# Kernel tuning notes

Hardware: AMD Instinct MI355X
Metric: run time of the kernel (lower is better)

Reference implementation:

```python
import jax, jax.numpy as jnp
import numpy as np

N = 10                 # n_wires
DIM = 1 << N           # Hilbert space dim = 1024
OPS = [''.join('Z' if i == j else 'I' for i in range(N)) for j in range(N)] + \
      [p + 'I' * (N - 2) for p in ['XX', 'YY', 'ZZ', 'XY', 'XZ', 'YZ']]

C64 = jnp.complex64
CNOT = jnp.array([[1, 0, 0, 0], [0, 1, 0, 0], [0, 0, 0, 1], [0, 0, 1, 0]], dtype=C64)
PAULI = {'X': jnp.array([[0, 1], [1, 0]], dtype=C64),
         'Y': jnp.array([[0, -1j], [1j, 0]], dtype=C64),
         'Z': jnp.array([[1, 0], [0, -1]], dtype=C64)}


def _rx(theta):
    c = jnp.cos(theta / 2).astype(C64)
    s = jnp.sin(theta / 2).astype(C64)
    return jnp.stack([jnp.stack([c, -1j * s]), jnp.stack([-1j * s, c])])


def _ry(theta):
    c = jnp.cos(theta / 2).astype(C64)
    s = jnp.sin(theta / 2).astype(C64)
    return jnp.stack([jnp.stack([c, -s]), jnp.stack([s, c])])


def _apply_gate(U, gate, qubits):
    """Left-multiply U by gate expanded onto `qubits` (little-endian: qubit 0 = LSB
    of the row index), without materializing the 2^N x 2^N expanded operator.
    Equivalent to expand_operator(gate, qubits, N) @ U."""
    k = len(qubits)
    T = U.reshape((2,) * N + (DIM,))          # row bit b <-> axis N-1-b
    src = tuple(N - 1 - q for q in reversed(qubits))  # MSB of gate index first
    T = jnp.moveaxis(T, src, tuple(range(k)))
    shp = T.shape
    T = (gate @ T.reshape(1 << k, -1)).reshape(shp)
    T = jnp.moveaxis(T, tuple(range(k)), src)
    return T.reshape(DIM, DIM)


def _build_unitary(rx0, ry0, ry1):
    U = jnp.eye(DIM, dtype=C64)
    for j in range(N):                         # local RY0 @ RX0 on each qubit
        U = _apply_gate(U, _ry(ry0[j]) @ _rx(rx0[j]), [j])
    for _ in range(N):                         # N entangling layers
        for j in range(N):
            U = _apply_gate(U, CNOT, [j, (j + 1) % N])
        for j in range(N):
            U = _apply_gate(U, _ry(ry1[j]), [j])
    return U


def _apply_pauli(states, p, q):
    """states: (BT,) + (2,)*N with qubit q at axis 1 + (N-1-q)."""
    ax = 1 + (N - 1 - q)
    s = jnp.moveaxis(states, ax, -1)
    s = jnp.einsum('ab,...b->...a', p, s)
    return jnp.moveaxis(s, -1, ax)


def setup_inputs() -> dict:
    key = jax.random.key(0)
    kx, k1, k2, k3 = jax.random.split(key, 4)
    x = jax.random.normal(kx, (16, 1024, 1024), dtype=jnp.float32)
    pi = np.float32(np.pi)
    rx0 = jax.random.uniform(k1, (N,), minval=-pi, maxval=pi, dtype=jnp.float32)
    ry0 = jax.random.uniform(k2, (N,), minval=-pi, maxval=pi, dtype=jnp.float32)
    ry1 = jax.random.uniform(k3, (N,), minval=-pi, maxval=pi, dtype=jnp.float32)
    return {"x": x, "rx0": rx0, "ry0": ry0, "ry1": ry1}


def reference(x, rx0, ry0, ry1):
    B, T, C = x.shape
    U = _build_unitary(rx0, ry0, ry1)
    xf = x.reshape(B * T, C)
    # amplitude encoding: L2-normalize each row onto the 2^N state
    psi = (xf / jnp.linalg.norm(xf, axis=-1, keepdims=True)).astype(C64)
    psi_out = psi @ U.T                        # (BT, DIM)
    phi0 = psi_out.reshape((B * T,) + (2,) * N)
    evs = []
    for op in OPS:
        phi = phi0
        for q, ch in enumerate(op):
            if ch != 'I':
                phi = _apply_pauli(phi, PAULI[ch], q)
        evs.append(jnp.sum(jnp.real(jnp.conj(phi0) * phi),
                           axis=tuple(range(1, N + 1))))
    out = jnp.stack(evs, axis=-1)              # (BT, hidden_dim)
    return out.reshape(B, T, len(OPS)).astype(jnp.float32)
```

## Files before the change

### kernel.cpp

```cpp
#include <hip/hip_runtime.h>

#define DIM 1024

typedef _Float16 half8  __attribute__((ext_vector_type(8)));
typedef _Float16 half4v __attribute__((ext_vector_type(4)));
typedef float    f32x4  __attribute__((ext_vector_type(4)));

#define LO_SCALE   2048.0f
#define LO_INV     4.8828125e-4f

__device__ __forceinline__ int swz(int p) { return p ^ ((p >> 4) & 15); }

__device__ __forceinline__ void gl2lds(const _Float16* g, _Float16* s) {
  __builtin_amdgcn_global_load_lds(
      (const __attribute__((address_space(1))) void*)g,
      (__attribute__((address_space(3))) void*)s, 16, 0, 0);
}

__global__ __launch_bounds__(256) void k_build(
    const float* __restrict__ rx0, const float* __restrict__ ry0,
    const float* __restrict__ ry1, _Float16* __restrict__ BtH,
    _Float16* __restrict__ BtL) {
  __shared__ float2 st[2][4][DIM];
  __shared__ unsigned short invp[DIM];
  __shared__ float2 rot[30];
  const int t = threadIdx.x;
  const int w = t >> 6;
  const int l = t & 63;
  const int k0 = blockIdx.x * 4;

  if (t < 30) {
    float th = (t < 10) ? rx0[t] : (t < 20 ? ry0[t - 10] : ry1[t - 20]);
    rot[t] = make_float2(cosf(0.5f * th), sinf(0.5f * th));
  }
  for (int p = t; p < DIM; p += 256) {
    int b = p;
    #pragma unroll
    for (int j = 9; j >= 0; --j) b ^= ((b >> ((j + 1) % 10)) & 1) << j;
    invp[p] = (unsigned short)b;
  }
  {
    const int k = k0 + w;
    for (int i = 0; i < 16; ++i) {
      int p = l * 16 + i;
      st[0][w][swz(p)] = make_float2(p == k ? 1.f : 0.f, 0.f);
    }
  }
  __syncthreads();

  int cur = 0;

  auto quad = [&](int qbase, bool ph1, bool gather) {
    float2 v[16];
    #pragma unroll
    for (int i = 0; i < 16; ++i) {
      int p = (qbase == 0) ? ((l << 4) | i)
                           : (((l >> 4) << 8) | (i << 4) | (l & 15));
      int sp = gather ? (int)invp[p] : p;
      v[i] = st[cur][w][swz(sp)];
    }
    #pragma unroll
    for (int qq = 0; qq < 4; ++qq) {
      const int q = qbase + qq;
      if (ph1) {
        const float cx = rot[q].x, sx = rot[q].y;
        #pragma unroll
        for (int i = 0; i < 16; ++i) {
          if (i & (1 << qq)) continue;
          const int j = i | (1 << qq);
          float2 a = v[i], b = v[j];
          v[i] = make_float2(cx*a.x + sx*b.y,  cx*a.y - sx*b.x);
          v[j] = make_float2(sx*a.y + cx*b.x, -sx*a.x + cx*b.y);
        }
      }
      const float cy = ph1 ? rot[10+q].x : rot[20+q].x;
      const float sy = ph1 ? rot[10+q].y : rot[20+q].y;
      #pragma unroll
      for (int i = 0; i < 16; ++i) {
        if (i & (1 << qq)) continue;
        const int j = i | (1 << qq);
        float2 a = v[i], b = v[j];
        v[i] = make_float2(cy*a.x - sy*b.x, cy*a.y - sy*b.y);
        v[j] = make_float2(sy*a.x + cy*b.x, sy*a.y + cy*b.y);
      }
    }
    const int dst = gather ? (cur ^ 1) : cur;
    #pragma unroll
    for (int i = 0; i < 16; ++i) {
      int p = (qbase == 0) ? ((l << 4) | i)
                           : (((l >> 4) << 8) | (i << 4) | (l & 15));
      st[dst][w][swz(p)] = v[i];
    }
    if (gather) cur ^= 1;
    __syncthreads();
  };

  auto duo = [&](bool ph1) {
    #pragma unroll
    for (int rep = 0; rep < 4; ++rep) {
      const int u = l + rep * 64;
      float2 v[4];
      #pragma unroll
      for (int i = 0; i < 4; ++i) v[i] = st[cur][w][swz((i << 8) | u)];
      #pragma unroll
      for (int qq = 0; qq < 2; ++qq) {
        const int q = 8 + qq;
        if (ph1) {
          const float cx = rot[q].x, sx = rot[q].y;
          #pragma unroll
          for (int i = 0; i < 4; ++i) {
            if (i & (1 << qq)) continue;
            const int j = i | (1 << qq);
            float2 a = v[i], b = v[j];
            v[i] = make_float2(cx*a.x + sx*b.y,  cx*a.y - sx*b.x);
            v[j] = make_float2(sx*a.y + cx*b.x, -sx*a.x + cx*b.y);
          }
        }
        const float cy = ph1 ? rot[10+q].x : rot[20+q].x;
        const float sy = ph1 ? rot[10+q].y : rot[20+q].y;
        #pragma unroll
        for (int i = 0; i < 4; ++i) {
          if (i & (1 << qq)) continue;
          const int j = i | (1 << qq);
          float2 a = v[i], b = v[j];
          v[i] = make_float2(cy*a.x - sy*b.x, cy*a.y - sy*b.y);
          v[j] = make_float2(sy*a.x + cy*b.x, sy*a.y + cy*b.y);
        }
      }
      #pragma unroll
      for (int i = 0; i < 4; ++i) st[cur][w][swz((i << 8) | u)] = v[i];
    }
    __syncthreads();
  };

  quad(0, true, false);  quad(4, true, false);  duo(true);
  for (int L = 0; L < 10; ++L) {
    quad(0, false, true);
    quad(4, false, false);
    duo(false);
  }

  for (int n = t; n < 2048; n += 256) {
    const int m = n >> 1;
    half4v hh, hl;
    #pragma unroll
    for (int c = 0; c < 4; ++c) {
      float2 a = st[cur][c][swz(m)];
      const float v = (n & 1) ? a.y : a.x;
      const _Float16 hi = (_Float16)v;
      hh[c] = hi;
      hl[c] = (_Float16)((v - (float)hi) * LO_SCALE);
    }
    *(half4v*)(BtH + (size_t)n * DIM + k0) = hh;
    *(half4v*)(BtL + (size_t)n * DIM + k0) = hl;
  }
}

__global__ __launch_bounds__(256) void k_norms(const float* __restrict__ x,
                                               float* __restrict__ invn) {
  const int row = blockIdx.x * 4 + (threadIdx.x >> 6);
  const int l = threadIdx.x & 63;
  const float4* xp = (const float4*)(x + (size_t)row * DIM);
  float ss = 0.f;
  #pragma unroll
  for (int i = 0; i < 4; ++i) {
    const float4 v = xp[l + i * 64];
    ss += v.x*v.x + v.y*v.y + v.z*v.z + v.w*v.w;
  }
  #pragma unroll
  for (int m = 32; m; m >>= 1) ss += __shfl_xor(ss, m);
  if (l == 0) invn[row] = rsqrtf(ss);
}

template <bool ATOMIC>
__global__ __launch_bounds__(256, 2) void k_gemm(
    const float* __restrict__ gA, const _Float16* __restrict__ gBh,
    const _Float16* __restrict__ gBl, const float* __restrict__ invn,
    float* __restrict__ partials, float* __restrict__ out) {
  __shared__ __align__(16) union SM {
    struct { _Float16 Ah[128][64], Al[128][64], Bh[128][64], Bl[128][64]; } s;
    struct { float C[128][65]; float ev[128][16]; } e;
  } sm;
  const int t = threadIdx.x;
  const int w = t >> 6, l = t & 63;
  const int wm = w & 1, wn = w >> 1;
  const int bid = blockIdx.x;
  const int bm = bid & 127, bn = bid >> 7;

  f32x4 accH[4][4] = {};
  f32x4 accC[4][4] = {};

  const int arow = bm*128 + (t >> 1);
  const float s = invn[arow];
  const float* aRow = gA + (size_t)arow*DIM + (t & 1)*32;
  const int ar = t >> 1;
  const int acb = (t & 1)*4;
  const size_t bOff = ((size_t)(bn*128 + w*32 + (l>>3)))*DIM + (((l&7)^(l>>3))*8);
  const _Float16* bSrcH = gBh + bOff;
  const _Float16* bSrcL = gBl + bOff;
  _Float16* bDstH = &sm.s.Bh[w*32][0];
  _Float16* bDstL = &sm.s.Bl[w*32][0];

  for (int kt = 0; kt < 16; ++kt) {
    #pragma unroll
    for (int i = 0; i < 4; ++i) {
      gl2lds(bSrcH + (size_t)i*8*DIM + kt*64, bDstH + i*8*64);
      gl2lds(bSrcL + (size_t)i*8*DIM + kt*64, bDstL + i*8*64);
    }
    {
      const float4* ap = (const float4*)(aRow + kt*64);
      float4 f[8];
      #pragma unroll
      for (int i = 0; i < 8; ++i) f[i] = ap[i];
      #pragma unroll
      for (int i = 0; i < 4; ++i) {
        float a[8] = { f[2*i].x*s, f[2*i].y*s, f[2*i].z*s, f[2*i].w*s,
                       f[2*i+1].x*s, f[2*i+1].y*s, f[2*i+1].z*s, f[2*i+1].w*s };
        half8 hh, hl;
        #pragma unroll
        for (int j = 0; j < 8; ++j) {
          const _Float16 hi = (_Float16)a[j];
          hh[j] = hi;
          hl[j] = (_Float16)((a[j] - (float)hi) * LO_SCALE);
        }
        const int c = ((acb + i) ^ (ar & 7)) * 8;
        *(half8*)&sm.s.Ah[ar][c] = hh;
        *(half8*)&sm.s.Al[ar][c] = hl;
      }
    }
    __syncthreads();
    #pragma unroll
    for (int ks = 0; ks < 2; ++ks) {
      half8 afh[4], afl[4], bfh[4], bfl[4];
      #pragma unroll
      for (int mi = 0; mi < 4; ++mi) {
        const int r = wm*64 + mi*16 + (l&15);
        const int c = ((ks*4 + (l>>4)) ^ (l&7)) * 8;
        afh[mi] = *(const half8*)&sm.s.Ah[r][c];
        afl[mi] = *(const half8*)&sm.s.Al[r][c];
      }
      #pragma unroll
      for (int ni = 0; ni < 4; ++ni) {
        const int r = wn*64 + ni*16 + (l&15);
        const int c = ((ks*4 + (l>>4)) ^ (l&7)) * 8;
        bfh[ni] = *(const half8*)&sm.s.Bh[r][c];
        bfl[ni] = *(const half8*)&sm.s.Bl[r][c];
      }
      #pragma unroll
      for (int mi = 0; mi < 4; ++mi)
        #pragma unroll
        for (int ni = 0; ni < 4; ++ni) {
          accH[mi][ni] = __builtin_amdgcn_mfma_f32_16x16x32_f16(
              afh[mi], bfh[ni], accH[mi][ni], 0, 0, 0);
          accC[mi][ni] = __builtin_amdgcn_mfma_f32_16x16x32_f16(
              afl[mi], bfh[ni], accC[mi][ni], 0, 0, 0);
          accC[mi][ni] = __builtin_amdgcn_mfma_f32_16x16x32_f16(
              afh[mi], bfl[ni], accC[mi][ni], 0, 0, 0);
        }
    }
    __syncthreads();
  }

  float ev[16];
  #pragma unroll
  for (int e = 0; e < 16; ++e) ev[e] = 0.f;
  const int er = t & 127, eh = t >> 7;

  #pragma unroll
  for (int chunk = 0; chunk < 2; ++chunk) {
    if (wn == chunk) {
      #pragma unroll
      for (int mi = 0; mi < 4; ++mi)
        #pragma unroll
        for (int ni = 0; ni < 4; ++ni)
          #pragma unroll
          for (int r = 0; r < 4; ++r)
            sm.e.C[wm*64 + mi*16 + (l>>4)*4 + r][ni*16 + (l&15)] =
                accH[mi][ni][r] + LO_INV * accC[mi][ni][r];
    }
    __syncthreads();
    #pragma unroll
    for (int gi = 0; gi < 4; ++gi) {
      const int g = eh*4 + gi;
      const float* cr = &sm.e.C[er][g*8];
      float yr0=cr[0], yi0=cr[1], yr1=cr[2], yi1=cr[3];
      float yr2=cr[4], yi2=cr[5], yr3=cr[6], yi3=cr[7];
      float n0=yr0*yr0+yi0*yi0, n1=yr1*yr1+yi1*yi1;
      float n2=yr2*yr2+yi2*yi2, n3=yr3*yr3+yi3*yi3;
      float p03r=yr0*yr3+yi0*yi3, p03i=yr0*yi3-yi0*yr3;
      float p12r=yr1*yr2+yi1*yi2, p12i=yr1*yi2-yi1*yr2;
      float p01r=yr0*yr1+yi0*yi1, p01i=yr0*yi1-yi0*yr1;
      float p23r=yr2*yr3+yi2*yi3, p23i=yr2*yi3-yi2*yr3;
      float ns = n0+n1+n2+n3;
      const int m0 = bn*64 + chunk*32 + g*4;
      ev[0]  += n0 - n1 + n2 - n3;
      ev[1]  += n0 + n1 - n2 - n3;
      #pragma unroll
      for (int q = 2; q < 10; ++q) ev[q] += ((m0 >> q) & 1) ? -ns : ns;
      ev[10] += 2.f*(p03r + p12r);
      ev[11] += 2.f*(p12r - p03r);
      ev[12] += n0 - n1 - n2 + n3;
      ev[13] += 2.f*(p03i + p12i);
      ev[14] += 2.f*(p01r - p23r);
      ev[15] += 2.f*(p01i - p23i);
    }
    __syncthreads();
  }
  if (eh == 1) {
    #pragma unroll
    for (int e = 0; e < 16; ++e) sm.e.ev[er][e] = ev[e];
  }
  __syncthreads();
  if (eh == 0) {
    const int row = bm*128 + er;
    if (ATOMIC) {
      #pragma unroll
      for (int e = 0; e < 16; ++e)
        atomicAdd(out + (size_t)row*16 + e, ev[e] + sm.e.ev[er][e]);
    } else {
      float* dst = partials + ((size_t)row*16 + bn)*16;
      #pragma unroll
      for (int e = 0; e < 16; ++e) dst[e] = ev[e] + sm.e.ev[er][e];
    }
  }
}

__global__ __launch_bounds__(256) void k_red(const float* __restrict__ partials,
                                             float* __restrict__ out) {
  const int gid = blockIdx.x * 256 + threadIdx.x;
  const int row = gid >> 4;
  float s = 0.f;
  #pragma unroll
  for (int bn = 0; bn < 16; ++bn) s += partials[((size_t)row*16 + bn)*16 + (gid & 15)];
  out[gid] = s;
}

extern "C" void kernel_launch(void* const* d_in, const int* in_sizes, int n_in,
                              void* d_out, int out_size, void* d_ws, size_t ws_size,
                              hipStream_t stream) {
  const float* x   = (const float*)d_in[0];
  const float* rx0 = (const float*)d_in[1];
  const float* ry0 = (const float*)d_in[2];
  const float* ry1 = (const float*)d_in[3];
  float* out = (float*)d_out;
  char* ws = (char*)d_ws;
  _Float16* BtH   = (_Float16*)ws;
  _Float16* BtL   = (_Float16*)(ws + ((size_t)4 << 20));
  float*    invn  = (float*)(ws + ((size_t)8 << 20));
  float*    partials = (float*)(ws + ((size_t)9 << 20));
  const bool part = ws_size >= ((size_t)25 << 20);

  k_build<<<dim3(256),  dim3(256), 0, stream>>>(rx0, ry0, ry1, BtH, BtL);
  k_norms<<<dim3(4096), dim3(256), 0, stream>>>(x, invn);
  if (part) {
    k_gemm<false><<<dim3(2048), dim3(256), 0, stream>>>(x, BtH, BtL, invn, partials, out);
    k_red<<<dim3(1024), dim3(256), 0, stream>>>(partials, out);
  } else {
    hipMemsetAsync(out, 0, (size_t)out_size * sizeof(float), stream);
    k_gemm<true><<<dim3(2048), dim3(256), 0, stream>>>(x, BtH, BtL, invn, partials, out);
  }
}
```

Baseline: 280.7 us.

## Double-buffer GEMM LDS tiles and use 512-thread blocks with 8 waves

The GEMM kernel now keeps two LDS buffers for the A and B tiles. It prefetches the next k-tile's global loads and writes its split-fp16 A conversion while MFMAs run on the current buffer, which removes one barrier per iteration and hides load latency. Blocks grow from 4 to 8 waves, each wave now computing a 64x32 subtile, and the epilogue reduces expectation values across four thread groups. The cost is double the LDS footprint (128KB for the tiles), which may limit occupancy, plus more redundant A-fragment reads across waves.

```diff
diff --git a/kernel.cpp b/kernel.cpp
--- a/kernel.cpp
+++ b/kernel.cpp
@@ -173,115 +173,124 @@
 }
 
 template <bool ATOMIC>
-__global__ __launch_bounds__(256, 2) void k_gemm(
+__global__ __launch_bounds__(512, 2) void k_gemm(
     const float* __restrict__ gA, const _Float16* __restrict__ gBh,
     const _Float16* __restrict__ gBl, const float* __restrict__ invn,
     float* __restrict__ partials, float* __restrict__ out) {
   __shared__ __align__(16) union SM {
-    struct { _Float16 Ah[128][64], Al[128][64], Bh[128][64], Bl[128][64]; } s;
-    struct { float C[128][65]; float ev[128][16]; } e;
+    struct { _Float16 Ah[2][128][64], Al[2][128][64],
+                      Bh[2][128][64], Bl[2][128][64]; } s;
+    struct { float C[128][65]; float ev[3][128][16]; } e;
   } sm;
   const int t = threadIdx.x;
   const int w = t >> 6, l = t & 63;
-  const int wm = w & 1, wn = w >> 1;
+  const int wm = w >> 2, wn = w & 3;
   const int bid = blockIdx.x;
   const int bm = bid & 127, bn = bid >> 7;
 
-  f32x4 accH[4][4] = {};
-  f32x4 accC[4][4] = {};
-
-  const int arow = bm*128 + (t >> 1);
+  f32x4 accH[4][2] = {};
+  f32x4 accC[4][2] = {};
+
+  const int ar = t >> 2, aq = t & 3;
+  const int arow = bm*128 + ar;
   const float s = invn[arow];
-  const float* aRow = gA + (size_t)arow*DIM + (t & 1)*32;
-  const int ar = t >> 1;
-  const int acb = (t & 1)*4;
-  const size_t bOff = ((size_t)(bn*128 + w*32 + (l>>3)))*DIM + (((l&7)^(l>>3))*8);
+  const float* aRow = gA + (size_t)arow*DIM + aq*16;
+  const size_t bOff = ((size_t)(bn*128 + w*16 + (l>>3)))*DIM + (((l&7)^(l>>3))*8);
   const _Float16* bSrcH = gBh + bOff;
   const _Float16* bSrcL = gBl + bOff;
-  _Float16* bDstH = &sm.s.Bh[w*32][0];
-  _Float16* bDstL = &sm.s.Bl[w*32][0];
-
+
+  float4 f[4];
+  auto stage_loads = [&](int kt) {
+    const float4* ap = (const float4*)(aRow + kt*64);
+    #pragma unroll
+    for (int i = 0; i < 4; ++i) f[i] = ap[i];
+  };
+  auto stage_b = [&](int kt, int d) {
+    #pragma unroll
+    for (int i = 0; i < 2; ++i) {
+      gl2lds(bSrcH + (size_t)i*8*DIM + kt*64, &sm.s.Bh[d][w*16 + i*8][0]);
+      gl2lds(bSrcL + (size_t)i*8*DIM + kt*64, &sm.s.Bl[d][w*16 + i*8][0]);
+    }
+  };
+  auto stage_a_write = [&](int d) {
+    #pragma unroll
+    for (int i = 0; i < 2; ++i) {
+      float a[8] = { f[2*i].x*s, f[2*i].y*s, f[2*i].z*s, f[2*i].w*s,
+                     f[2*i+1].x*s, f[2*i+1].y*s, f[2*i+1].z*s, f[2*i+1].w*s };
+      half8 hh, hl;
+      #pragma unroll
+      for (int j = 0; j < 8; ++j) {
+        const _Float16 hi = (_Float16)a[j];
+        hh[j] = hi;
+        hl[j] = (_Float16)((a[j] - (float)hi) * LO_SCALE);
+      }
+      const int c = ((aq*2 + i) ^ (ar & 7)) * 8;
+      *(half8*)&sm.s.Ah[d][ar][c] = hh;
+      *(half8*)&sm.s.Al[d][ar][c] = hl;
+    }
+  };
+  auto compute_ks = [&](int d, int ks) {
+    const int c = ((ks*4 + (l>>4)) ^ (l&7)) * 8;
+    half8 afh[4], afl[4], bfh[2], bfl[2];
+    #pragma unroll
+    for (int mi = 0; mi < 4; ++mi) {
+      const int r = wm*64 + mi*16 + (l&15);
+      afh[mi] = *(const half8*)&sm.s.Ah[d][r][c];
+      afl[mi] = *(const half8*)&sm.s.Al[d][r][c];
+    }
+    #pragma unroll
+    for (int ni = 0; ni < 2; ++ni) {
+      const int r = wn*32 + ni*16 + (l&15);
+      bfh[ni] = *(const half8*)&sm.s.Bh[d][r][c];
+      bfl[ni] = *(const half8*)&sm.s.Bl[d][r][c];
+    }
+    #pragma unroll
+    for (int mi = 0; mi < 4; ++mi)
+      #pragma unroll
+      for (int ni = 0; ni < 2; ++ni) {
+        accH[mi][ni] = __builtin_amdgcn_mfma_f32_16x16x32_f16(
+            afh[mi], bfh[ni], accH[mi][ni], 0, 0, 0);
+        accC[mi][ni] = __builtin_amdgcn_mfma_f32_16x16x32_f16(
+            afl[mi], bfh[ni], accC[mi][ni], 0, 0, 0);
+        accC[mi][ni] = __builtin_amdgcn_mfma_f32_16x16x32_f16(
+            afh[mi], bfl[ni], accC[mi][ni], 0, 0, 0);
+      }
+  };
+
+  stage_loads(0); stage_b(0, 0); stage_a_write(0);
+  __syncthreads();
+
+  #pragma unroll 2
   for (int kt = 0; kt < 16; ++kt) {
-    #pragma unroll
-    for (int i = 0; i < 4; ++i) {
-      gl2lds(bSrcH + (size_t)i*8*DIM + kt*64, bDstH + i*8*64);
-      gl2lds(bSrcL + (size_t)i*8*DIM + kt*64, bDstL + i*8*64);
-    }
-    {
-      const float4* ap = (const float4*)(aRow + kt*64);
-      float4 f[8];
-      #pragma unroll
-      for (int i = 0; i < 8; ++i) f[i] = ap[i];
-      #pragma unroll
-      for (int i = 0; i < 4; ++i) {
-        float a[8] = { f[2*i].x*s, f[2*i].y*s, f[2*i].z*s, f[2*i].w*s,
-                       f[2*i+1].x*s, f[2*i+1].y*s, f[2*i+1].z*s, f[2*i+1].w*s };
-        half8 hh, hl;
-        #pragma unroll
-        for (int j = 0; j < 8; ++j) {
-          const _Float16 hi = (_Float16)a[j];
-          hh[j] = hi;
-          hl[j] = (_Float16)((a[j] - (float)hi) * LO_SCALE);
-        }
-        const int c = ((acb + i) ^ (ar & 7)) * 8;
-        *(half8*)&sm.s.Ah[ar][c] = hh;
-        *(half8*)&sm.s.Al[ar][c] = hl;
-      }
-    }
-    __syncthreads();
-    #pragma unroll
-    for (int ks = 0; ks < 2; ++ks) {
-      half8 afh[4], afl[4], bfh[4], bfl[4];
-      #pragma unroll
-      for (int mi = 0; mi < 4; ++mi) {
-        const int r = wm*64 + mi*16 + (l&15);
-        const int c = ((ks*4 + (l>>4)) ^ (l&7)) * 8;
-        afh[mi] = *(const half8*)&sm.s.Ah[r][c];
-        afl[mi] = *(const half8*)&sm.s.Al[r][c];
-      }
-      #pragma unroll
-      for (int ni = 0; ni < 4; ++ni) {
-        const int r = wn*64 + ni*16 + (l&15);
-        const int c = ((ks*4 + (l>>4)) ^ (l&7)) * 8;
-        bfh[ni] = *(const half8*)&sm.s.Bh[r][c];
-        bfl[ni] = *(const half8*)&sm.s.Bl[r][c];
-      }
+    const int cur = kt & 1;
+    if (kt < 15) { stage_loads(kt + 1); stage_b(kt + 1, cur ^ 1); }
+    compute_ks(cur, 0);
+    if (kt < 15) stage_a_write(cur ^ 1);
+    compute_ks(cur, 1);
+    __syncthreads();
+  }
+
+  float ev[16];
+  #pragma unroll
+  for (int e = 0; e < 16; ++e) ev[e] = 0.f;
+  const int er = t & 127, eh = t >> 7;
+
+  #pragma unroll
+  for (int ch = 0; ch < 2; ++ch) {
+    if ((wn >> 1) == ch) {
       #pragma unroll
       for (int mi = 0; mi < 4; ++mi)
         #pragma unroll
-        for (int ni = 0; ni < 4; ++ni) {
-          accH[mi][ni] = __builtin_amdgcn_mfma_f32_16x16x32_f16(
-              afh[mi], bfh[ni], accH[mi][ni], 0, 0, 0);
-          accC[mi][ni] = __builtin_amdgcn_mfma_f32_16x16x32_f16(
-              afl[mi], bfh[ni], accC[mi][ni], 0, 0, 0);
-          accC[mi][ni] = __builtin_amdgcn_mfma_f32_16x16x32_f16(
-              afh[mi], bfl[ni], accC[mi][ni], 0, 0, 0);
-        }
-    }
-    __syncthreads();
-  }
-
-  float ev[16];
-  #pragma unroll
-  for (int e = 0; e < 16; ++e) ev[e] = 0.f;
-  const int er = t & 127, eh = t >> 7;
-
-  #pragma unroll
-  for (int chunk = 0; chunk < 2; ++chunk) {
-    if (wn == chunk) {
-      #pragma unroll
-      for (int mi = 0; mi < 4; ++mi)
-        #pragma unroll
-        for (int ni = 0; ni < 4; ++ni)
+        for (int ni = 0; ni < 2; ++ni)
           #pragma unroll
           for (int r = 0; r < 4; ++r)
-            sm.e.C[wm*64 + mi*16 + (l>>4)*4 + r][ni*16 + (l&15)] =
+            sm.e.C[wm*64 + mi*16 + (l>>4)*4 + r][(wn&1)*32 + ni*16 + (l&15)] =
                 accH[mi][ni][r] + LO_INV * accC[mi][ni][r];
     }
     __syncthreads();
     #pragma unroll
-    for (int gi = 0; gi < 4; ++gi) {
-      const int g = eh*4 + gi;
+    for (int gi = 0; gi < 2; ++gi) {
+      const int g = eh*2 + gi;
       const float* cr = &sm.e.C[er][g*8];
       float yr0=cr[0], yi0=cr[1], yr1=cr[2], yi1=cr[3];
       float yr2=cr[4], yi2=cr[5], yr3=cr[6], yi3=cr[7];
@@ -292,7 +301,7 @@
       float p01r=yr0*yr1+yi0*yi1, p01i=yr0*yi1-yi0*yr1;
       float p23r=yr2*yr3+yi2*yi3, p23i=yr2*yi3-yi2*yr3;
       float ns = n0+n1+n2+n3;
-      const int m0 = bn*64 + chunk*32 + g*4;
+      const int m0 = bn*64 + ch*32 + g*4;
       ev[0]  += n0 - n1 + n2 - n3;
       ev[1]  += n0 + n1 - n2 - n3;
       #pragma unroll
@@ -306,21 +315,19 @@
     }
     __syncthreads();
   }
-  if (eh == 1) {
-    #pragma unroll
-    for (int e = 0; e < 16; ++e) sm.e.ev[er][e] = ev[e];
+  if (eh > 0) {
+    #pragma unroll
+    for (int e = 0; e < 16; ++e) sm.e.ev[eh-1][er][e] = ev[e];
   }
   __syncthreads();
   if (eh == 0) {
     const int row = bm*128 + er;
-    if (ATOMIC) {
-      #pragma unroll
-      for (int e = 0; e < 16; ++e)
-        atomicAdd(out + (size_t)row*16 + e, ev[e] + sm.e.ev[er][e]);
-    } else {
-      float* dst = partials + ((size_t)row*16 + bn)*16;
-      #pragma unroll
-      for (int e = 0; e < 16; ++e) dst[e] = ev[e] + sm.e.ev[er][e];
+    #pragma unroll
+    for (int e = 0; e < 16; ++e) {
+      const float tot = ev[e] + sm.e.ev[0][er][e] + sm.e.ev[1][er][e]
+                      + sm.e.ev[2][er][e];
+      if (ATOMIC) atomicAdd(out + (size_t)row*16 + e, tot);
+      else        partials[((size_t)row*16 + bn)*16 + e] = tot;
     }
   }
 }
@@ -353,10 +360,10 @@
   k_build<<<dim3(256),  dim3(256), 0, stream>>>(rx0, ry0, ry1, BtH, BtL);
   k_norms<<<dim3(4096), dim3(256), 0, stream>>>(x, invn);
   if (part) {
-    k_gemm<false><<<dim3(2048), dim3(256), 0, stream>>>(x, BtH, BtL, invn, partials, out);
+    k_gemm<false><<<dim3(2048), dim3(512), 0, stream>>>(x, BtH, BtL, invn, partials, out);
     k_red<<<dim3(1024), dim3(256), 0, stream>>>(partials, out);
   } else {
     hipMemsetAsync(out, 0, (size_t)out_size * sizeof(float), stream);
-    k_gemm<true><<<dim3(2048), dim3(256), 0, stream>>>(x, BtH, BtL, invn, partials, out);
-  }
-}
+    k_gemm<true><<<dim3(2048), dim3(512), 0, stream>>>(x, BtH, BtL, invn, partials, out);
+  }
+}
```

After: 315.0 us. 1.12x slower.
